# Kernel tuning notes

Measured on AMD Instinct MI355X. Metric: run time of the kernel, lower is better.

Reference implementation:

```python
import jax, jax.numpy as jnp
import numpy as np

B, S, D, H, L, V = 4, 1000, 512, 8, 4, 32000
HD = D // H
FF = 4 * D
EPS = 1e-5


def setup_inputs() -> dict:
    key = jax.random.key(0)
    ks = jax.random.split(key, 24)
    s = 0.02
    inp = {
        'tokens': jax.random.randint(ks[0], (B, S), 0, V, dtype=jnp.int32),
        'emb': jax.random.normal(ks[1], (V, D), jnp.float32) * s,
        'wq': jax.random.normal(ks[2], (L, D, D), jnp.float32) * s,
        'bq': jnp.zeros((L, D), jnp.float32),
        'wk': jax.random.normal(ks[3], (L, D, D), jnp.float32) * s,
        'bk': jnp.zeros((L, D), jnp.float32),
        'wv': jax.random.normal(ks[4], (L, D, D), jnp.float32) * s,
        'bv': jnp.zeros((L, D), jnp.float32),
        'wo': jax.random.normal(ks[5], (L, D, D), jnp.float32) * s,
        'bo': jnp.zeros((L, D), jnp.float32),
        'ln1_g': jnp.ones((L, D), jnp.float32),
        'ln1_b': jnp.zeros((L, D), jnp.float32),
        'w1': jax.random.normal(ks[6], (L, D, FF), jnp.float32) * s,
        'b1': jnp.zeros((L, FF), jnp.float32),
        'w2': jax.random.normal(ks[7], (L, FF, D), jnp.float32) * s,
        'b2': jnp.zeros((L, D), jnp.float32),
        'ln2_g': jnp.ones((L, D), jnp.float32),
        'ln2_b': jnp.zeros((L, D), jnp.float32),
        'fc_w': jax.random.normal(ks[8], (D, V), jnp.float32) * s,
        'fc_b': jnp.zeros((V,), jnp.float32),
    }
    return inp


def _layernorm(x, g, b):
    mu = jnp.mean(x, axis=-1, keepdims=True)
    var = jnp.mean(jnp.square(x - mu), axis=-1, keepdims=True)
    return (x - mu) * jax.lax.rsqrt(var + EPS) * g + b


def _pos_encoding(seq_len, dim):
    pos = jnp.arange(seq_len, dtype=jnp.float32)[:, None]
    div = jnp.exp(jnp.arange(0, dim, 2, dtype=jnp.float32) * (-np.log(10000.0) / dim))
    pe = jnp.zeros((seq_len, dim), jnp.float32)
    pe = pe.at[:, 0::2].set(jnp.sin(pos * div))
    pe = pe.at[:, 1::2].set(jnp.cos(pos * div))
    return pe


def reference(tokens, emb, wq, bq, wk, bk, wv, bv, wo, bo,
              ln1_g, ln1_b, w1, b1, w2, b2, ln2_g, ln2_b, fc_w, fc_b):
    x = emb[tokens]                      # [B,S,D]
    x = x + _pos_encoding(S, D)
    scale = 1.0 / np.sqrt(HD)
    for i in range(L):
        # multi-head attention (unfused, as in source)
        q = (x @ wq[i] + bq[i]).reshape(B, S, H, HD).transpose(0, 2, 1, 3)
        k = (x @ wk[i] + bk[i]).reshape(B, S, H, HD).transpose(0, 2, 1, 3)
        v = (x @ wv[i] + bv[i]).reshape(B, S, H, HD).transpose(0, 2, 1, 3)
        scores = jnp.einsum('bhqd,bhkd->bhqk', q, k) * scale  # [B,H,S,S]
        attn = jax.nn.softmax(scores, axis=-1)
        ctx = jnp.einsum('bhqk,bhkd->bhqd', attn, v)
        ctx = ctx.transpose(0, 2, 1, 3).reshape(B, S, D)
        attended = ctx @ wo[i] + bo[i]
        x = _layernorm(x + attended, ln1_g[i], ln1_b[i])
        # feed-forward
        h = jax.nn.relu(x @ w1[i] + b1[i])
        ff = h @ w2[i] + b2[i]
        x = _layernorm(x + ff, ln2_g[i], ln2_b[i])
    logits = x @ fc_w + fc_b             # [B,S,V]
    return jax.nn.softmax(logits, axis=-1)
```

## Files before the change

kernel.cpp:

```cpp
#include <hip/hip_runtime.h>
#include <math.h>

#define BB 4
#define SS 1000
#define DD 512
#define HH 8
#define HD 64
#define LL 4
#define FFD 2048
#define VV 32000
#define MM (BB*SS)
#define QKV_STR 1536

typedef __attribute__((ext_vector_type(8))) short bf16x8;
typedef __attribute__((ext_vector_type(4))) short bf16x4;
typedef __attribute__((ext_vector_type(4))) float f32x4;

__device__ __forceinline__ unsigned short f2bf(float f)
{
    unsigned int u = __float_as_uint(f);
    u += 0x7FFFu + ((u >> 16) & 1u);
    return (unsigned short)(u >> 16);
}
__device__ __forceinline__ float bf2f(unsigned short h)
{
    return __uint_as_float((unsigned int)h << 16);
}
__device__ __forceinline__ void cvt8(const float* f, unsigned int* hp, unsigned int* lp)
{
#pragma unroll
    for (int j = 0; j < 4; j++) {
        unsigned short h0 = f2bf(f[2 * j]);
        unsigned short h1 = f2bf(f[2 * j + 1]);
        unsigned short l0 = f2bf(f[2 * j] - bf2f(h0));
        unsigned short l1 = f2bf(f[2 * j + 1] - bf2f(h1));
        hp[j] = (unsigned int)h0 | ((unsigned int)h1 << 16);
        lp[j] = (unsigned int)l0 | ((unsigned int)l1 << 16);
    }
}
__device__ __forceinline__ void split8(const float* f, bf16x8& h8, bf16x8& l8)
{
#pragma unroll
    for (int j = 0; j < 8; j++) {
        unsigned short h = f2bf(f[j]);
        unsigned short l = f2bf(f[j] - bf2f(h));
        h8[j] = (short)h;
        l8[j] = (short)l;
    }
}

__global__ __launch_bounds__(256) void embed_pe_kernel(
    const int* __restrict__ tokens, const float* __restrict__ emb,
    float* __restrict__ x)
{
    int idx = blockIdx.x * 256 + threadIdx.x;
    int d  = idx & (DD - 1);
    int bs = idx >> 9;
    int s  = bs % SS;
    int tok = tokens[bs];
    float i2 = (float)(d & ~1);
    float dv = expf(i2 * (-9.210340371976184f / (float)DD));
    float ang = (float)s * dv;
    float pe = (d & 1) ? cosf(ang) : sinf(ang);
    x[idx] = emb[(size_t)tok * DD + d] + pe;
}

#define BKP 40

__device__ __forceinline__ void gemm_core(
    const float* __restrict__ A, const float* __restrict__ W, int ldw, int wcol,
    const float* __restrict__ bias, float* __restrict__ C, int ldc, int ccol,
    int M, int K, int relu, int bm)
{
    __shared__ unsigned short Ah[128][BKP];
    __shared__ unsigned short Al[128][BKP];
    __shared__ unsigned short Bh[128][BKP];
    __shared__ unsigned short Bl[128][BKP];

    const int tid  = threadIdx.x;
    const int lane = tid & 63;
    const int wid  = tid >> 6;
    const int wm   = (wid >> 1) << 6;
    const int wn   = (wid & 1) << 6;
    const int fr   = lane & 15;
    const int ko   = (lane >> 4) << 3;

    const int am  = tid >> 2;
    const int aks = (tid & 3) << 3;
    const int bn  = tid & 63;
    const int bkk = (tid >> 6) << 3;

    f32x4 acc[4][4];
#pragma unroll
    for (int i = 0; i < 4; i++)
#pragma unroll
        for (int j = 0; j < 4; j++)
            acc[i][j] = (f32x4){0.f, 0.f, 0.f, 0.f};

    for (int k0 = 0; k0 < K; k0 += 32) {
#pragma unroll
        for (int u = 0; u < 2; u++) {
            const int m  = am + (u << 6);
            const int gm = bm + m;
            float fv[8];
            if (gm < M) {
                const float* ap = &A[(size_t)gm * K + k0 + aks];
                float4 x0 = *(const float4*)ap;
                float4 x1 = *(const float4*)(ap + 4);
                fv[0] = x0.x; fv[1] = x0.y; fv[2] = x0.z; fv[3] = x0.w;
                fv[4] = x1.x; fv[5] = x1.y; fv[6] = x1.z; fv[7] = x1.w;
            } else {
#pragma unroll
                for (int j = 0; j < 8; j++) fv[j] = 0.f;
            }
            unsigned int hp[4], lp[4];
            cvt8(fv, hp, lp);
            *(uint4*)&Ah[m][aks] = make_uint4(hp[0], hp[1], hp[2], hp[3]);
            *(uint4*)&Al[m][aks] = make_uint4(lp[0], lp[1], lp[2], lp[3]);
        }
#pragma unroll
        for (int u = 0; u < 2; u++) {
            const int n = bn + (u << 6);
            const float* wp = &W[(size_t)(k0 + bkk) * ldw + wcol + n];
            float fv[8];
#pragma unroll
            for (int i = 0; i < 8; i++) fv[i] = wp[(size_t)i * ldw];
            unsigned int hp[4], lp[4];
            cvt8(fv, hp, lp);
            *(uint4*)&Bh[n][bkk] = make_uint4(hp[0], hp[1], hp[2], hp[3]);
            *(uint4*)&Bl[n][bkk] = make_uint4(lp[0], lp[1], lp[2], lp[3]);
        }
        __syncthreads();

        bf16x8 ah[4], al[4], bh[4], bl[4];
#pragma unroll
        for (int i = 0; i < 4; i++) {
            ah[i] = *(const bf16x8*)&Ah[wm + i * 16 + fr][ko];
            al[i] = *(const bf16x8*)&Al[wm + i * 16 + fr][ko];
        }
#pragma unroll
        for (int j = 0; j < 4; j++) {
            bh[j] = *(const bf16x8*)&Bh[wn + j * 16 + fr][ko];
            bl[j] = *(const bf16x8*)&Bl[wn + j * 16 + fr][ko];
        }
#pragma unroll
        for (int i = 0; i < 4; i++)
#pragma unroll
            for (int j = 0; j < 4; j++) {
                acc[i][j] = __builtin_amdgcn_mfma_f32_16x16x32_bf16(ah[i], bh[j], acc[i][j], 0, 0, 0);
                acc[i][j] = __builtin_amdgcn_mfma_f32_16x16x32_bf16(ah[i], bl[j], acc[i][j], 0, 0, 0);
                acc[i][j] = __builtin_amdgcn_mfma_f32_16x16x32_bf16(al[i], bh[j], acc[i][j], 0, 0, 0);
            }
        __syncthreads();
    }

    const int cr = (lane >> 4) << 2;
    const int cc = lane & 15;
#pragma unroll
    for (int j = 0; j < 4; j++) {
        const int lc  = wn + j * 16 + cc;
        const float bv = bias[wcol + lc];
        const int col = ccol + lc;
#pragma unroll
        for (int i = 0; i < 4; i++) {
            f32x4 a = acc[i][j];
#pragma unroll
            for (int r = 0; r < 4; r++) {
                const int row = bm + wm + i * 16 + cr + r;
                if (row < M) {
                    float v = a[r] + bv;
                    if (relu) v = fmaxf(v, 0.f);
                    C[(size_t)row * ldc + col] = v;
                }
            }
        }
    }
}

__global__ __launch_bounds__(256) void gemm_mfma_kernel(
    const float* __restrict__ A, const float* __restrict__ W,
    const float* __restrict__ bias, float* __restrict__ C,
    int M, int N, int K, int relu)
{
    const int bm   = blockIdx.y * 128;
    const int wcol = blockIdx.x * 128;
    gemm_core(A, W, N, wcol, bias, C, N, wcol, M, K, relu, bm);
}

__global__ __launch_bounds__(256) void gemm_qkv_kernel(
    const float* __restrict__ A,
    const float* __restrict__ wq, const float* __restrict__ wk, const float* __restrict__ wv,
    const float* __restrict__ bq, const float* __restrict__ bk, const float* __restrict__ bv,
    float* __restrict__ qkv, int M)
{
    const int bm   = blockIdx.y * 128;
    const int bx   = blockIdx.x;
    const int sel  = bx >> 2;
    const int wcol = (bx & 3) << 7;
    const int ccol = bx << 7;
    const float* W  = (sel == 0) ? wq : (sel == 1) ? wk : wv;
    const float* bi = (sel == 0) ? bq : (sel == 1) ? bk : bv;
    gemm_core(A, W, DD, wcol, bi, qkv, QKV_STR, ccol, M, DD, 0, bm);
}

#define QT 128
#define KVT 64
#define KP 72
#define VP 72

__device__ __forceinline__ bf16x8 ld_pair(const unsigned short* p0,
                                          const unsigned short* p1)
{
    union { bf16x8 v; bf16x4 q[2]; } u;
    u.q[0] = *(const bf16x4*)p0;
    u.q[1] = *(const bf16x4*)p1;
    return u.v;
}

__global__ __launch_bounds__(512) void attention_kernel(
    const float* __restrict__ qkv, float* __restrict__ ctx)
{
    __shared__ __align__(16) unsigned short Kh[KVT][KP];
    __shared__ __align__(16) unsigned short Kl[KVT][KP];
    __shared__ __align__(16) unsigned short Vth[HD][VP];
    __shared__ __align__(16) unsigned short Vtl[HD][VP];

    const int tid  = threadIdx.x;
    const int lane = tid & 63;
    const int w    = tid >> 6;
    const int r16  = lane & 15;
    const int g    = lane >> 4;

    const int nqt = (SS + QT - 1) / QT;
    const int qt  = blockIdx.x % nqt;
    const int bh  = blockIdx.x / nqt;
    const int h   = bh % HH;
    const int b   = bh / HH;
    const int q0  = qt * QT;

    const size_t base = (size_t)b * SS * QKV_STR + (size_t)h * HD;

    const int qrow = q0 + w * 16 + r16;
    const int qr   = qrow < SS ? qrow : SS - 1;
    const float* qp = qkv + base + (size_t)qr * QKV_STR;
    bf16x8 qh[2], ql[2];
#pragma unroll
    for (int c = 0; c < 2; c++) {
        float4 qa = *(const float4*)&qp[c * 32 + g * 4];
        float4 qb = *(const float4*)&qp[c * 32 + 16 + g * 4];
        float fv[8] = {qa.x * 0.125f, qa.y * 0.125f, qa.z * 0.125f, qa.w * 0.125f,
                       qb.x * 0.125f, qb.y * 0.125f, qb.z * 0.125f, qb.w * 0.125f};
        split8(fv, qh[c], ql[c]);
    }

    f32x4 oacc[4];
#pragma unroll
    for (int f = 0; f < 4; f++) oacc[f] = (f32x4){0.f, 0.f, 0.f, 0.f};
    float mrow = -1e30f, lrow = 0.f;

    const int ntiles = (SS + KVT - 1) / KVT;
    for (int t = 0; t < ntiles; t++) {
        const int kv0 = t * KVT;
        __syncthreads();
        {
            const int kj   = tid >> 3;
            const int dblk = (tid & 7) * 8;
            float fv[8];
            const int krow = kv0 + kj;
            if (krow < SS) {
                const float* kp = qkv + base + (size_t)krow * QKV_STR + DD;
                float4 a0 = *(const float4*)&kp[dblk];
                float4 a1 = *(const float4*)&kp[dblk + 4];
                fv[0] = a0.x; fv[1] = a0.y; fv[2] = a0.z; fv[3] = a0.w;
                fv[4] = a1.x; fv[5] = a1.y; fv[6] = a1.z; fv[7] = a1.w;
            } else {
#pragma unroll
                for (int j = 0; j < 8; j++) fv[j] = 0.f;
            }
            bf16x8 h8, l8;
            split8(fv, h8, l8);
            *(bf16x8*)&Kh[kj][dblk] = h8;
            *(bf16x8*)&Kl[kj][dblk] = l8;
        }
        {
            const int kj = tid & 63;
            const int d0 = (tid >> 6) * 8;
            float fv[8];
            const int vrow = kv0 + kj;
            if (vrow < SS) {
                const float* vp = qkv + base + (size_t)vrow * QKV_STR + 2 * DD;
                float4 a0 = *(const float4*)&vp[d0];
                float4 a1 = *(const float4*)&vp[d0 + 4];
                fv[0] = a0.x; fv[1] = a0.y; fv[2] = a0.z; fv[3] = a0.w;
                fv[4] = a1.x; fv[5] = a1.y; fv[6] = a1.z; fv[7] = a1.w;
            } else {
#pragma unroll
                for (int j = 0; j < 8; j++) fv[j] = 0.f;
            }
#pragma unroll
            for (int i = 0; i < 8; i++) {
                unsigned short hh = f2bf(fv[i]);
                unsigned short ll = f2bf(fv[i] - bf2f(hh));
                Vth[d0 + i][kj] = hh;
                Vtl[d0 + i][kj] = ll;
            }
        }
        __syncthreads();

        f32x4 sac[4];
#pragma unroll
        for (int f = 0; f < 4; f++) sac[f] = (f32x4){0.f, 0.f, 0.f, 0.f};
#pragma unroll
        for (int f = 0; f < 4; f++) {
            const int ar = f * 16 + r16;
#pragma unroll
            for (int c = 0; c < 2; c++) {
                bf16x8 ah = ld_pair(&Kh[ar][c * 32 + g * 4], &Kh[ar][c * 32 + 16 + g * 4]);
                bf16x8 al = ld_pair(&Kl[ar][c * 32 + g * 4], &Kl[ar][c * 32 + 16 + g * 4]);
                sac[f] = __builtin_amdgcn_mfma_f32_16x16x32_bf16(ah, qh[c], sac[f], 0, 0, 0);
                sac[f] = __builtin_amdgcn_mfma_f32_16x16x32_bf16(ah, ql[c], sac[f], 0, 0, 0);
                sac[f] = __builtin_amdgcn_mfma_f32_16x16x32_bf16(al, qh[c], sac[f], 0, 0, 0);
            }
        }
        if (kv0 + KVT > SS) {
#pragma unroll
            for (int f = 0; f < 4; f++)
#pragma unroll
                for (int rr = 0; rr < 4; rr++)
                    if (kv0 + f * 16 + g * 4 + rr >= SS) sac[f][rr] = -1e30f;
        }

        float tmax = -1e30f;
#pragma unroll
        for (int f = 0; f < 4; f++)
#pragma unroll
            for (int rr = 0; rr < 4; rr++) tmax = fmaxf(tmax, sac[f][rr]);
        tmax = fmaxf(tmax, __shfl_xor(tmax, 16));
        tmax = fmaxf(tmax, __shfl_xor(tmax, 32));
        const float mnew = fmaxf(mrow, tmax);
        const float scal = __expf(mrow - mnew);
        mrow = mnew;
        float tsum = 0.f;
#pragma unroll
        for (int f = 0; f < 4; f++)
#pragma unroll
            for (int rr = 0; rr < 4; rr++) {
                float e = __expf(sac[f][rr] - mnew);
                sac[f][rr] = e;
                tsum += e;
            }
        tsum += __shfl_xor(tsum, 16);
        tsum += __shfl_xor(tsum, 32);
        lrow = lrow * scal + tsum;
#pragma unroll
        for (int f = 0; f < 4; f++) {
            oacc[f][0] *= scal; oacc[f][1] *= scal;
            oacc[f][2] *= scal; oacc[f][3] *= scal;
        }

        bf16x8 ph[2], pl[2];
#pragma unroll
        for (int c = 0; c < 2; c++) {
            float pv[8] = {sac[2 * c][0], sac[2 * c][1], sac[2 * c][2], sac[2 * c][3],
                           sac[2 * c + 1][0], sac[2 * c + 1][1], sac[2 * c + 1][2], sac[2 * c + 1][3]};
            split8(pv, ph[c], pl[c]);
        }

#pragma unroll
        for (int f = 0; f < 4; f++) {
            const int ar = f * 16 + r16;
#pragma unroll
            for (int c = 0; c < 2; c++) {
                bf16x8 vh = ld_pair(&Vth[ar][c * 32 + g * 4], &Vth[ar][c * 32 + 16 + g * 4]);
                bf16x8 vl = ld_pair(&Vtl[ar][c * 32 + g * 4], &Vtl[ar][c * 32 + 16 + g * 4]);
                oacc[f] = __builtin_amdgcn_mfma_f32_16x16x32_bf16(vh, ph[c], oacc[f], 0, 0, 0);
                oacc[f] = __builtin_amdgcn_mfma_f32_16x16x32_bf16(vh, pl[c], oacc[f], 0, 0, 0);
                oacc[f] = __builtin_amdgcn_mfma_f32_16x16x32_bf16(vl, ph[c], oacc[f], 0, 0, 0);
            }
        }
    }

    if (qrow < SS) {
        const float inv = 1.f / lrow;
        float* cp = ctx + ((size_t)b * SS + qrow) * DD + (size_t)h * HD;
#pragma unroll
        for (int f = 0; f < 4; f++) {
            float4 o;
            o.x = oacc[f][0] * inv;
            o.y = oacc[f][1] * inv;
            o.z = oacc[f][2] * inv;
            o.w = oacc[f][3] * inv;
            *(float4*)&cp[f * 16 + g * 4] = o;
        }
    }
}

__global__ __launch_bounds__(128) void add_ln_kernel(
    float* __restrict__ x, const float* __restrict__ res,
    const float* __restrict__ g, const float* __restrict__ bta)
{
    const int row = blockIdx.x;
    const int tid = threadIdx.x;
    float* xr = x + (size_t)row * DD;
    const float* rr = res + (size_t)row * DD;

    float4 xv = ((const float4*)xr)[tid];
    float4 rv = ((const float4*)rr)[tid];
    xv.x += rv.x; xv.y += rv.y; xv.z += rv.z; xv.w += rv.w;

    __shared__ float red1[2];
    __shared__ float red2[2];
    const int lane = tid & 63;
    const int w = tid >> 6;

    float s = xv.x + xv.y + xv.z + xv.w;
#pragma unroll
    for (int off = 32; off > 0; off >>= 1) s += __shfl_xor(s, off);
    if (lane == 0) red1[w] = s;
    __syncthreads();
    const float mean = (red1[0] + red1[1]) * (1.f / (float)DD);

    float d0 = xv.x - mean, d1 = xv.y - mean, d2 = xv.z - mean, d3 = xv.w - mean;
    float sq = d0 * d0 + d1 * d1 + d2 * d2 + d3 * d3;
#pragma unroll
    for (int off = 32; off > 0; off >>= 1) sq += __shfl_xor(sq, off);
    if (lane == 0) red2[w] = sq;
    __syncthreads();
    const float inv = 1.f / sqrtf((red2[0] + red2[1]) * (1.f / (float)DD) + 1e-5f);

    float4 gv = ((const float4*)g)[tid];
    float4 bv = ((const float4*)bta)[tid];
    float4 o;
    o.x = d0 * inv * gv.x + bv.x;
    o.y = d1 * inv * gv.y + bv.y;
    o.z = d2 * inv * gv.z + bv.z;
    o.w = d3 * inv * gv.w + bv.w;
    ((float4*)xr)[tid] = o;
}

__global__ __launch_bounds__(256) void softmax_kernel(float* __restrict__ out)
{
    const int row = blockIdx.x;
    float* p = out + (size_t)row * VV;
    const int tid = threadIdx.x;

    float m = -1e30f, s = 0.f;
    for (int j = tid * 4; j < VV; j += 1024) {
        float4 c = *(const float4*)&p[j];
        float lm = fmaxf(fmaxf(c.x, c.y), fmaxf(c.z, c.w));
        if (lm > m) { s *= expf(m - lm); m = lm; }
        s += expf(c.x - m) + expf(c.y - m) + expf(c.z - m) + expf(c.w - m);
    }
#pragma unroll
    for (int off = 32; off > 0; off >>= 1) {
        float mo = __shfl_xor(m, off);
        float so = __shfl_xor(s, off);
        float nm = fmaxf(m, mo);
        s = s * expf(m - nm) + so * expf(mo - nm);
        m = nm;
    }
    __shared__ float ms[4], ss2[4];
    const int lane = tid & 63;
    const int w = tid >> 6;
    if (lane == 0) { ms[w] = m; ss2[w] = s; }
    __syncthreads();
    float fm = fmaxf(fmaxf(ms[0], ms[1]), fmaxf(ms[2], ms[3]));
    float fs = ss2[0] * expf(ms[0] - fm) + ss2[1] * expf(ms[1] - fm) +
               ss2[2] * expf(ms[2] - fm) + ss2[3] * expf(ms[3] - fm);
    const float inv = 1.f / fs;
    for (int j = tid * 4; j < VV; j += 1024) {
        float4 c = *(const float4*)&p[j];
        c.x = expf(c.x - fm) * inv;
        c.y = expf(c.y - fm) * inv;
        c.z = expf(c.z - fm) * inv;
        c.w = expf(c.w - fm) * inv;
        *(float4*)&p[j] = c;
    }
}

static inline void launch_gemm(const float* A, const float* W, const float* bias,
                               float* C, int M, int N, int K, int relu,
                               hipStream_t st)
{
    dim3 grid(N / 128, (M + 127) / 128);
    gemm_mfma_kernel<<<grid, 256, 0, st>>>(A, W, bias, C, M, N, K, relu);
}

extern "C" void kernel_launch(void* const* d_in, const int* in_sizes, int n_in,
                              void* d_out, int out_size, void* d_ws, size_t ws_size,
                              hipStream_t stream)
{
    const int*   tokens = (const int*)  d_in[0];
    const float* emb    = (const float*)d_in[1];
    const float* wq     = (const float*)d_in[2];
    const float* bq     = (const float*)d_in[3];
    const float* wk     = (const float*)d_in[4];
    const float* bk     = (const float*)d_in[5];
    const float* wv     = (const float*)d_in[6];
    const float* bv     = (const float*)d_in[7];
    const float* wo     = (const float*)d_in[8];
    const float* bo     = (const float*)d_in[9];
    const float* ln1g   = (const float*)d_in[10];
    const float* ln1b   = (const float*)d_in[11];
    const float* w1     = (const float*)d_in[12];
    const float* b1     = (const float*)d_in[13];
    const float* w2     = (const float*)d_in[14];
    const float* b2     = (const float*)d_in[15];
    const float* ln2g   = (const float*)d_in[16];
    const float* ln2b   = (const float*)d_in[17];
    const float* fcw    = (const float*)d_in[18];
    const float* fcb    = (const float*)d_in[19];
    float* out = (float*)d_out;

    const size_t XN = (size_t)MM * DD;
    float* x    = (float*)d_ws;
    float* qkv  = x   + XN;
    float* ctx  = qkv + 3 * XN;
    float* attn = ctx + XN;
    float* hbuf = out + ((size_t)MM * VV - (size_t)MM * FFD);

    embed_pe_kernel<<<(MM * DD) / 256, 256, 0, stream>>>(tokens, emb, x);

    for (int l = 0; l < LL; l++) {
        const size_t wo2 = (size_t)l * DD * DD;
        gemm_qkv_kernel<<<dim3(12, (MM + 127) / 128), 256, 0, stream>>>(
            x, wq + wo2, wk + wo2, wv + wo2,
            bq + l * DD, bk + l * DD, bv + l * DD, qkv, MM);
        attention_kernel<<<BB * HH * ((SS + QT - 1) / QT), 512, 0, stream>>>(qkv, ctx);
        launch_gemm(ctx, wo + wo2, bo + l * DD, attn, MM, DD, DD, 0, stream);
        add_ln_kernel<<<MM, 128, 0, stream>>>(x, attn, ln1g + l * DD, ln1b + l * DD);
        launch_gemm(x, w1 + (size_t)l * DD * FFD, b1 + l * FFD, hbuf, MM, FFD, DD, 1, stream);
        launch_gemm(hbuf, w2 + (size_t)l * FFD * DD, b2 + l * DD, attn, MM, DD, FFD, 0, stream);
        add_ln_kernel<<<MM, 128, 0, stream>>>(x, attn, ln2g + l * DD, ln2b + l * DD);
    }

    launch_gemm(x, fcw, fcb, out, MM, VV, DD, 0, stream);
    softmax_kernel<<<MM, 256, 0, stream>>>(out);
}
```

Measured before the change: 2.942 ms.

## Pre-split activations and weights to bf16 hi/lo, drop split for final projection

Producers (embedding, layernorm, GEMM epilogues, attention) now write bf16 hi/lo pairs directly, and weights are pre-transposed and split by a separate conversion kernel. GEMMs and attention load bf16 tiles straight into shared memory instead of converting fp32 on every tile load. The large vocabulary projection now uses a single bf16 MFMA pass with bf16-only activations instead of the 3-term split. This removes repeated conversion work and the strided weight reads, but the output GEMM loses the lo correction terms, which lowers logits precision.

```diff
diff --git a/kernel.cpp b/kernel.cpp
--- a/kernel.cpp
+++ b/kernel.cpp
@@ -26,18 +26,6 @@
 {
     return __uint_as_float((unsigned int)h << 16);
 }
-__device__ __forceinline__ void cvt8(const float* f, unsigned int* hp, unsigned int* lp)
-{
-#pragma unroll
-    for (int j = 0; j < 4; j++) {
-        unsigned short h0 = f2bf(f[2 * j]);
-        unsigned short h1 = f2bf(f[2 * j + 1]);
-        unsigned short l0 = f2bf(f[2 * j] - bf2f(h0));
-        unsigned short l1 = f2bf(f[2 * j + 1] - bf2f(h1));
-        hp[j] = (unsigned int)h0 | ((unsigned int)h1 << 16);
-        lp[j] = (unsigned int)l0 | ((unsigned int)l1 << 16);
-    }
-}
 __device__ __forceinline__ void split8(const float* f, bf16x8& h8, bf16x8& l8)
 {
 #pragma unroll
@@ -51,7 +39,8 @@
 
 __global__ __launch_bounds__(256) void embed_pe_kernel(
     const int* __restrict__ tokens, const float* __restrict__ emb,
-    float* __restrict__ x)
+    float* __restrict__ x, unsigned short* __restrict__ xhi,
+    unsigned short* __restrict__ xlo)
 {
     int idx = blockIdx.x * 256 + threadIdx.x;
     int d  = idx & (DD - 1);
@@ -62,20 +51,76 @@
     float dv = expf(i2 * (-9.210340371976184f / (float)DD));
     float ang = (float)s * dv;
     float pe = (d & 1) ? cosf(ang) : sinf(ang);
-    x[idx] = emb[(size_t)tok * DD + d] + pe;
+    float v = emb[(size_t)tok * DD + d] + pe;
+    x[idx] = v;
+    unsigned short h = f2bf(v);
+    xhi[idx] = h;
+    xlo[idx] = f2bf(v - bf2f(h));
+}
+
+__global__ __launch_bounds__(256) void wtconv_kernel(
+    const float* __restrict__ W, int ldn,
+    unsigned short* __restrict__ thi, unsigned short* __restrict__ tlo,
+    int ldk, int n0)
+{
+    __shared__ unsigned short lh[32][33];
+    __shared__ unsigned short ll[32][33];
+    const int tid = threadIdx.x;
+    const int nn0 = blockIdx.x * 32;
+    const int k0  = blockIdx.y * 32;
+
+    {
+        const int k = tid >> 3;
+        const int n = (tid & 7) * 4;
+        float4 v = *(const float4*)&W[(size_t)(k0 + k) * ldn + nn0 + n];
+        float fv[4] = {v.x, v.y, v.z, v.w};
+#pragma unroll
+        for (int i = 0; i < 4; i++) {
+            unsigned short h = f2bf(fv[i]);
+            lh[k][n + i] = h;
+            ll[k][n + i] = f2bf(fv[i] - bf2f(h));
+        }
+    }
+    __syncthreads();
+    {
+        const int nw = tid >> 3;
+        const int kw = (tid & 7) * 4;
+        unsigned int h0 = (unsigned int)lh[kw][nw]     | ((unsigned int)lh[kw + 1][nw] << 16);
+        unsigned int h1 = (unsigned int)lh[kw + 2][nw] | ((unsigned int)lh[kw + 3][nw] << 16);
+        unsigned int l0 = (unsigned int)ll[kw][nw]     | ((unsigned int)ll[kw + 1][nw] << 16);
+        unsigned int l1 = (unsigned int)ll[kw + 2][nw] | ((unsigned int)ll[kw + 3][nw] << 16);
+        const size_t o = (size_t)(n0 + nn0 + nw) * ldk + k0 + kw;
+        *(uint2*)&thi[o] = make_uint2(h0, h1);
+        *(uint2*)&tlo[o] = make_uint2(l0, l1);
+    }
+}
+
+__global__ __launch_bounds__(256) void concat_bias_kernel(
+    const float* __restrict__ a, const float* __restrict__ b,
+    const float* __restrict__ c, float* __restrict__ o)
+{
+    int t = blockIdx.x * 256 + threadIdx.x;
+    if (t < 512) o[t] = a[t];
+    else if (t < 1024) o[t] = b[t - 512];
+    else if (t < 1536) o[t] = c[t - 1024];
 }
 
 #define BKP 40
 
-__device__ __forceinline__ void gemm_core(
-    const float* __restrict__ A, const float* __restrict__ W, int ldw, int wcol,
-    const float* __restrict__ bias, float* __restrict__ C, int ldc, int ccol,
-    int M, int K, int relu, int bm)
+template<int SPLIT, bool BF32, bool OSPLIT>
+__global__ __launch_bounds__(256) void gemm_t(
+    const unsigned short* __restrict__ Ahi, const unsigned short* __restrict__ Alo,
+    const unsigned short* __restrict__ Bth, const unsigned short* __restrict__ Btl,
+    const float* __restrict__ Bf, int ldbf,
+    const float* __restrict__ bias,
+    float* __restrict__ Cf, unsigned short* __restrict__ Chi,
+    unsigned short* __restrict__ Clo,
+    int M, int K, int ldc, int relu)
 {
     __shared__ unsigned short Ah[128][BKP];
-    __shared__ unsigned short Al[128][BKP];
+    __shared__ unsigned short Al[SPLIT == 3 ? 128 : 1][SPLIT == 3 ? BKP : 1];
     __shared__ unsigned short Bh[128][BKP];
-    __shared__ unsigned short Bl[128][BKP];
+    __shared__ unsigned short Bl[SPLIT == 3 ? 128 : 1][SPLIT == 3 ? BKP : 1];
 
     const int tid  = threadIdx.x;
     const int lane = tid & 63;
@@ -84,11 +129,8 @@
     const int wn   = (wid & 1) << 6;
     const int fr   = lane & 15;
     const int ko   = (lane >> 4) << 3;
-
-    const int am  = tid >> 2;
-    const int aks = (tid & 3) << 3;
-    const int bn  = tid & 63;
-    const int bkk = (tid >> 6) << 3;
+    const int bm   = blockIdx.y * 128;
+    const int bn0  = blockIdx.x * 128;
 
     f32x4 acc[4][4];
 #pragma unroll
@@ -97,59 +139,63 @@
         for (int j = 0; j < 4; j++)
             acc[i][j] = (f32x4){0.f, 0.f, 0.f, 0.f};
 
+    const uint4 zz = {0u, 0u, 0u, 0u};
     for (int k0 = 0; k0 < K; k0 += 32) {
 #pragma unroll
-        for (int u = 0; u < 2; u++) {
-            const int m  = am + (u << 6);
-            const int gm = bm + m;
-            float fv[8];
-            if (gm < M) {
-                const float* ap = &A[(size_t)gm * K + k0 + aks];
-                float4 x0 = *(const float4*)ap;
-                float4 x1 = *(const float4*)(ap + 4);
-                fv[0] = x0.x; fv[1] = x0.y; fv[2] = x0.z; fv[3] = x0.w;
-                fv[4] = x1.x; fv[5] = x1.y; fv[6] = x1.z; fv[7] = x1.w;
-            } else {
-#pragma unroll
-                for (int j = 0; j < 8; j++) fv[j] = 0.f;
-            }
-            unsigned int hp[4], lp[4];
-            cvt8(fv, hp, lp);
-            *(uint4*)&Ah[m][aks] = make_uint4(hp[0], hp[1], hp[2], hp[3]);
-            *(uint4*)&Al[m][aks] = make_uint4(lp[0], lp[1], lp[2], lp[3]);
-        }
-#pragma unroll
-        for (int u = 0; u < 2; u++) {
-            const int n = bn + (u << 6);
-            const float* wp = &W[(size_t)(k0 + bkk) * ldw + wcol + n];
-            float fv[8];
-#pragma unroll
-            for (int i = 0; i < 8; i++) fv[i] = wp[(size_t)i * ldw];
-            unsigned int hp[4], lp[4];
-            cvt8(fv, hp, lp);
-            *(uint4*)&Bh[n][bkk] = make_uint4(hp[0], hp[1], hp[2], hp[3]);
-            *(uint4*)&Bl[n][bkk] = make_uint4(lp[0], lp[1], lp[2], lp[3]);
+        for (int p = 0; p < 2; p++) {
+            const int c   = tid + (p << 8);
+            const int row = c >> 2;
+            const int ks  = (c & 3) << 3;
+            const int gm  = bm + row;
+            *(uint4*)&Ah[row][ks] =
+                (gm < M) ? *(const uint4*)&Ahi[(size_t)gm * K + k0 + ks] : zz;
+            if (SPLIT == 3)
+                *(uint4*)&Al[row][ks] =
+                    (gm < M) ? *(const uint4*)&Alo[(size_t)gm * K + k0 + ks] : zz;
+            if (!BF32) {
+                *(uint4*)&Bh[row][ks] = *(const uint4*)&Bth[(size_t)(bn0 + row) * K + k0 + ks];
+                if (SPLIT == 3)
+                    *(uint4*)&Bl[row][ks] = *(const uint4*)&Btl[(size_t)(bn0 + row) * K + k0 + ks];
+            }
+        }
+        if (BF32) {
+#pragma unroll
+            for (int u = 0; u < 2; u++) {
+                const int n   = (tid & 63) + (u << 6);
+                const int bkk = (tid >> 6) << 3;
+                const float* wp = &Bf[(size_t)(k0 + bkk) * ldbf + bn0 + n];
+                unsigned int hp[4];
+#pragma unroll
+                for (int i = 0; i < 4; i++) {
+                    unsigned short h0 = f2bf(wp[(size_t)(2 * i) * ldbf]);
+                    unsigned short h1 = f2bf(wp[(size_t)(2 * i + 1) * ldbf]);
+                    hp[i] = (unsigned int)h0 | ((unsigned int)h1 << 16);
+                }
+                *(uint4*)&Bh[n][bkk] = make_uint4(hp[0], hp[1], hp[2], hp[3]);
+            }
         }
         __syncthreads();
 
-        bf16x8 ah[4], al[4], bh[4], bl[4];
+        bf16x8 ah[4], bh[4], al[4], bl[4];
 #pragma unroll
         for (int i = 0; i < 4; i++) {
             ah[i] = *(const bf16x8*)&Ah[wm + i * 16 + fr][ko];
-            al[i] = *(const bf16x8*)&Al[wm + i * 16 + fr][ko];
+            if (SPLIT == 3) al[i] = *(const bf16x8*)&Al[wm + i * 16 + fr][ko];
         }
 #pragma unroll
         for (int j = 0; j < 4; j++) {
             bh[j] = *(const bf16x8*)&Bh[wn + j * 16 + fr][ko];
-            bl[j] = *(const bf16x8*)&Bl[wn + j * 16 + fr][ko];
+            if (SPLIT == 3) bl[j] = *(const bf16x8*)&Bl[wn + j * 16 + fr][ko];
         }
 #pragma unroll
         for (int i = 0; i < 4; i++)
 #pragma unroll
             for (int j = 0; j < 4; j++) {
                 acc[i][j] = __builtin_amdgcn_mfma_f32_16x16x32_bf16(ah[i], bh[j], acc[i][j], 0, 0, 0);
-                acc[i][j] = __builtin_amdgcn_mfma_f32_16x16x32_bf16(ah[i], bl[j], acc[i][j], 0, 0, 0);
-                acc[i][j] = __builtin_amdgcn_mfma_f32_16x16x32_bf16(al[i], bh[j], acc[i][j], 0, 0, 0);
+                if (SPLIT == 3) {
+                    acc[i][j] = __builtin_amdgcn_mfma_f32_16x16x32_bf16(ah[i], bl[j], acc[i][j], 0, 0, 0);
+                    acc[i][j] = __builtin_amdgcn_mfma_f32_16x16x32_bf16(al[i], bh[j], acc[i][j], 0, 0, 0);
+                }
             }
         __syncthreads();
     }
@@ -159,8 +205,8 @@
 #pragma unroll
     for (int j = 0; j < 4; j++) {
         const int lc  = wn + j * 16 + cc;
-        const float bv = bias[wcol + lc];
-        const int col = ccol + lc;
+        const float bv = bias[bn0 + lc];
+        const int col = bn0 + lc;
 #pragma unroll
         for (int i = 0; i < 4; i++) {
             f32x4 a = acc[i][j];
@@ -170,37 +216,17 @@
                 if (row < M) {
                     float v = a[r] + bv;
                     if (relu) v = fmaxf(v, 0.f);
-                    C[(size_t)row * ldc + col] = v;
+                    if (OSPLIT) {
+                        unsigned short h = f2bf(v);
+                        Chi[(size_t)row * ldc + col] = h;
+                        Clo[(size_t)row * ldc + col] = f2bf(v - bf2f(h));
+                    } else {
+                        Cf[(size_t)row * ldc + col] = v;
+                    }
                 }
             }
         }
     }
-}
-
-__global__ __launch_bounds__(256) void gemm_mfma_kernel(
-    const float* __restrict__ A, const float* __restrict__ W,
-    const float* __restrict__ bias, float* __restrict__ C,
-    int M, int N, int K, int relu)
-{
-    const int bm   = blockIdx.y * 128;
-    const int wcol = blockIdx.x * 128;
-    gemm_core(A, W, N, wcol, bias, C, N, wcol, M, K, relu, bm);
-}
-
-__global__ __launch_bounds__(256) void gemm_qkv_kernel(
-    const float* __restrict__ A,
-    const float* __restrict__ wq, const float* __restrict__ wk, const float* __restrict__ wv,
-    const float* __restrict__ bq, const float* __restrict__ bk, const float* __restrict__ bv,
-    float* __restrict__ qkv, int M)
-{
-    const int bm   = blockIdx.y * 128;
-    const int bx   = blockIdx.x;
-    const int sel  = bx >> 2;
-    const int wcol = (bx & 3) << 7;
-    const int ccol = bx << 7;
-    const float* W  = (sel == 0) ? wq : (sel == 1) ? wk : wv;
-    const float* bi = (sel == 0) ? bq : (sel == 1) ? bk : bv;
-    gemm_core(A, W, DD, wcol, bi, qkv, QKV_STR, ccol, M, DD, 0, bm);
 }
 
 #define QT 128
@@ -218,7 +244,8 @@
 }
 
 __global__ __launch_bounds__(512) void attention_kernel(
-    const float* __restrict__ qkv, float* __restrict__ ctx)
+    const unsigned short* __restrict__ qvh, const unsigned short* __restrict__ qvl,
+    unsigned short* __restrict__ chi, unsigned short* __restrict__ clo)
 {
     __shared__ __align__(16) unsigned short Kh[KVT][KP];
     __shared__ __align__(16) unsigned short Kl[KVT][KP];
@@ -242,15 +269,13 @@
 
     const int qrow = q0 + w * 16 + r16;
     const int qr   = qrow < SS ? qrow : SS - 1;
-    const float* qp = qkv + base + (size_t)qr * QKV_STR;
+    const unsigned short* qph = qvh + base + (size_t)qr * QKV_STR;
+    const unsigned short* qpl = qvl + base + (size_t)qr * QKV_STR;
     bf16x8 qh[2], ql[2];
 #pragma unroll
     for (int c = 0; c < 2; c++) {
-        float4 qa = *(const float4*)&qp[c * 32 + g * 4];
-        float4 qb = *(const float4*)&qp[c * 32 + 16 + g * 4];
-        float fv[8] = {qa.x * 0.125f, qa.y * 0.125f, qa.z * 0.125f, qa.w * 0.125f,
-                       qb.x * 0.125f, qb.y * 0.125f, qb.z * 0.125f, qb.w * 0.125f};
-        split8(fv, qh[c], ql[c]);
+        qh[c] = ld_pair(&qph[c * 32 + g * 4], &qph[c * 32 + 16 + g * 4]);
+        ql[c] = ld_pair(&qpl[c * 32 + g * 4], &qpl[c * 32 + 16 + g * 4]);
     }
 
     f32x4 oacc[4];
@@ -258,6 +283,7 @@
     for (int f = 0; f < 4; f++) oacc[f] = (f32x4){0.f, 0.f, 0.f, 0.f};
     float mrow = -1e30f, lrow = 0.f;
 
+    const uint4 zz = {0u, 0u, 0u, 0u};
     const int ntiles = (SS + KVT - 1) / KVT;
     for (int t = 0; t < ntiles; t++) {
         const int kv0 = t * KVT;
@@ -265,44 +291,32 @@
         {
             const int kj   = tid >> 3;
             const int dblk = (tid & 7) * 8;
-            float fv[8];
             const int krow = kv0 + kj;
             if (krow < SS) {
-                const float* kp = qkv + base + (size_t)krow * QKV_STR + DD;
-                float4 a0 = *(const float4*)&kp[dblk];
-                float4 a1 = *(const float4*)&kp[dblk + 4];
-                fv[0] = a0.x; fv[1] = a0.y; fv[2] = a0.z; fv[3] = a0.w;
-                fv[4] = a1.x; fv[5] = a1.y; fv[6] = a1.z; fv[7] = a1.w;
+                const size_t o = base + (size_t)krow * QKV_STR + DD + dblk;
+                *(uint4*)&Kh[kj][dblk] = *(const uint4*)&qvh[o];
+                *(uint4*)&Kl[kj][dblk] = *(const uint4*)&qvl[o];
             } else {
-#pragma unroll
-                for (int j = 0; j < 8; j++) fv[j] = 0.f;
-            }
-            bf16x8 h8, l8;
-            split8(fv, h8, l8);
-            *(bf16x8*)&Kh[kj][dblk] = h8;
-            *(bf16x8*)&Kl[kj][dblk] = l8;
+                *(uint4*)&Kh[kj][dblk] = zz;
+                *(uint4*)&Kl[kj][dblk] = zz;
+            }
         }
         {
             const int kj = tid & 63;
             const int d0 = (tid >> 6) * 8;
-            float fv[8];
             const int vrow = kv0 + kj;
+            union { uint4 u; unsigned short s[8]; } vh4, vl4;
             if (vrow < SS) {
-                const float* vp = qkv + base + (size_t)vrow * QKV_STR + 2 * DD;
-                float4 a0 = *(const float4*)&vp[d0];
-                float4 a1 = *(const float4*)&vp[d0 + 4];
-                fv[0] = a0.x; fv[1] = a0.y; fv[2] = a0.z; fv[3] = a0.w;
-                fv[4] = a1.x; fv[5] = a1.y; fv[6] = a1.z; fv[7] = a1.w;
+                const size_t o = base + (size_t)vrow * QKV_STR + 2 * DD + d0;
+                vh4.u = *(const uint4*)&qvh[o];
+                vl4.u = *(const uint4*)&qvl[o];
             } else {
-#pragma unroll
-                for (int j = 0; j < 8; j++) fv[j] = 0.f;
+                vh4.u = zz; vl4.u = zz;
             }
 #pragma unroll
             for (int i = 0; i < 8; i++) {
-                unsigned short hh = f2bf(fv[i]);
-                unsigned short ll = f2bf(fv[i] - bf2f(hh));
-                Vth[d0 + i][kj] = hh;
-                Vtl[d0 + i][kj] = ll;
+                Vth[d0 + i][kj] = vh4.s[i];
+                Vtl[d0 + i][kj] = vl4.s[i];
             }
         }
         __syncthreads();
@@ -322,6 +336,10 @@
                 sac[f] = __builtin_amdgcn_mfma_f32_16x16x32_bf16(al, qh[c], sac[f], 0, 0, 0);
             }
         }
+#pragma unroll
+        for (int f = 0; f < 4; f++)
+#pragma unroll
+            for (int rr = 0; rr < 4; rr++) sac[f][rr] *= 0.125f;
         if (kv0 + KVT > SS) {
 #pragma unroll
             for (int f = 0; f < 4; f++)
@@ -382,22 +400,30 @@
 
     if (qrow < SS) {
         const float inv = 1.f / lrow;
-        float* cp = ctx + ((size_t)b * SS + qrow) * DD + (size_t)h * HD;
+        const size_t ci = ((size_t)b * SS + qrow) * DD + (size_t)h * HD;
 #pragma unroll
         for (int f = 0; f < 4; f++) {
-            float4 o;
-            o.x = oacc[f][0] * inv;
-            o.y = oacc[f][1] * inv;
-            o.z = oacc[f][2] * inv;
-            o.w = oacc[f][3] * inv;
-            *(float4*)&cp[f * 16 + g * 4] = o;
+            unsigned short hs[4], ls[4];
+#pragma unroll
+            for (int r = 0; r < 4; r++) {
+                float v = oacc[f][r] * inv;
+                hs[r] = f2bf(v);
+                ls[r] = f2bf(v - bf2f(hs[r]));
+            }
+            unsigned int h0 = (unsigned int)hs[0] | ((unsigned int)hs[1] << 16);
+            unsigned int h1 = (unsigned int)hs[2] | ((unsigned int)hs[3] << 16);
+            unsigned int l0 = (unsigned int)ls[0] | ((unsigned int)ls[1] << 16);
+            unsigned int l1 = (unsigned int)ls[2] | ((unsigned int)ls[3] << 16);
+            *(uint2*)&chi[ci + f * 16 + g * 4] = make_uint2(h0, h1);
+            *(uint2*)&clo[ci + f * 16 + g * 4] = make_uint2(l0, l1);
         }
     }
 }
 
 __global__ __launch_bounds__(128) void add_ln_kernel(
     float* __restrict__ x, const float* __restrict__ res,
-    const float* __restrict__ g, const float* __restrict__ bta)
+    const float* __restrict__ g, const float* __restrict__ bta,
+    unsigned short* __restrict__ xhi, unsigned short* __restrict__ xlo)
 {
     const int row = blockIdx.x;
     const int tid = threadIdx.x;
@@ -436,6 +462,15 @@
     o.z = d2 * inv * gv.z + bv.z;
     o.w = d3 * inv * gv.w + bv.w;
     ((float4*)xr)[tid] = o;
+
+    unsigned short h0 = f2bf(o.x), h1 = f2bf(o.y), h2 = f2bf(o.z), h3 = f2bf(o.w);
+    unsigned short l0 = f2bf(o.x - bf2f(h0)), l1 = f2bf(o.y - bf2f(h1));
+    unsigned short l2 = f2bf(o.z - bf2f(h2)), l3 = f2bf(o.w - bf2f(h3));
+    const size_t oidx = (size_t)row * DD + tid * 4;
+    *(uint2*)&xhi[oidx] = make_uint2((unsigned int)h0 | ((unsigned int)h1 << 16),
+                                     (unsigned int)h2 | ((unsigned int)h3 << 16));
+    *(uint2*)&xlo[oidx] = make_uint2((unsigned int)l0 | ((unsigned int)l1 << 16),
+                                     (unsigned int)l2 | ((unsigned int)l3 << 16));
 }
 
 __global__ __launch_bounds__(256) void softmax_kernel(float* __restrict__ out)
@@ -476,14 +511,6 @@
         c.w = expf(c.w - fm) * inv;
         *(float4*)&p[j] = c;
     }
-}
-
-static inline void launch_gemm(const float* A, const float* W, const float* bias,
-                               float* C, int M, int N, int K, int relu,
-                               hipStream_t st)
-{
-    dim3 grid(N / 128, (M + 127) / 128);
-    gemm_mfma_kernel<<<grid, 256, 0, st>>>(A, W, bias, C, M, N, K, relu);
 }
 
 extern "C" void kernel_launch(void* const* d_in, const int* in_sizes, int n_in,
@@ -513,27 +540,57 @@
     float* out = (float*)d_out;
 
     const size_t XN = (size_t)MM * DD;
-    float* x    = (float*)d_ws;
-    float* qkv  = x   + XN;
-    float* ctx  = qkv + 3 * XN;
-    float* attn = ctx + XN;
-    float* hbuf = out + ((size_t)MM * VV - (size_t)MM * FFD);
-
-    embed_pe_kernel<<<(MM * DD) / 256, 256, 0, stream>>>(tokens, emb, x);
+    float* ws = (float*)d_ws;
+    float* x = ws;
+    unsigned short* xhi = (unsigned short*)(ws + XN);
+    unsigned short* xlo = xhi + XN;
+    unsigned short* qkvhi = (unsigned short*)(ws + 2 * XN);
+    unsigned short* qkvlo = qkvhi + 3 * XN;
+    float* attn = ws + 5 * XN;
+
+    unsigned short* tailu = (unsigned short*)(out + ((size_t)MM * VV - (size_t)MM * FFD));
+    unsigned short* ctxhi = tailu;
+    unsigned short* ctxlo = tailu + XN;
+    unsigned short* Hhi   = tailu;
+    unsigned short* Hlo   = tailu + (size_t)MM * FFD;
+
+    unsigned short* wth = qkvhi;
+    unsigned short* wtl = qkvhi + 1048576;
+    unsigned short* qwth = (unsigned short*)attn;
+    unsigned short* qwtl = qwth + 786432;
+    float* biasc = (float*)(qwtl + 786432);
+
+    embed_pe_kernel<<<(MM * DD) / 256, 256, 0, stream>>>(tokens, emb, x, xhi, xlo);
 
     for (int l = 0; l < LL; l++) {
         const size_t wo2 = (size_t)l * DD * DD;
-        gemm_qkv_kernel<<<dim3(12, (MM + 127) / 128), 256, 0, stream>>>(
-            x, wq + wo2, wk + wo2, wv + wo2,
-            bq + l * DD, bk + l * DD, bv + l * DD, qkv, MM);
-        attention_kernel<<<BB * HH * ((SS + QT - 1) / QT), 512, 0, stream>>>(qkv, ctx);
-        launch_gemm(ctx, wo + wo2, bo + l * DD, attn, MM, DD, DD, 0, stream);
-        add_ln_kernel<<<MM, 128, 0, stream>>>(x, attn, ln1g + l * DD, ln1b + l * DD);
-        launch_gemm(x, w1 + (size_t)l * DD * FFD, b1 + l * FFD, hbuf, MM, FFD, DD, 1, stream);
-        launch_gemm(hbuf, w2 + (size_t)l * FFD * DD, b2 + l * DD, attn, MM, DD, FFD, 0, stream);
-        add_ln_kernel<<<MM, 128, 0, stream>>>(x, attn, ln2g + l * DD, ln2b + l * DD);
-    }
-
-    launch_gemm(x, fcw, fcb, out, MM, VV, DD, 0, stream);
+        concat_bias_kernel<<<6, 256, 0, stream>>>(bq + l * DD, bk + l * DD, bv + l * DD, biasc);
+        wtconv_kernel<<<dim3(16, 16), 256, 0, stream>>>(wq + wo2, DD, qwth, qwtl, DD, 0);
+        wtconv_kernel<<<dim3(16, 16), 256, 0, stream>>>(wk + wo2, DD, qwth, qwtl, DD, 512);
+        wtconv_kernel<<<dim3(16, 16), 256, 0, stream>>>(wv + wo2, DD, qwth, qwtl, DD, 1024);
+        gemm_t<3, false, true><<<dim3(12, 32), 256, 0, stream>>>(
+            xhi, xlo, qwth, qwtl, nullptr, 0, biasc,
+            nullptr, qkvhi, qkvlo, MM, DD, QKV_STR, 0);
+        attention_kernel<<<BB * HH * ((SS + QT - 1) / QT), 512, 0, stream>>>(
+            qkvhi, qkvlo, ctxhi, ctxlo);
+        wtconv_kernel<<<dim3(16, 16), 256, 0, stream>>>(wo + wo2, DD, wth, wtl, DD, 0);
+        gemm_t<3, false, false><<<dim3(4, 32), 256, 0, stream>>>(
+            ctxhi, ctxlo, wth, wtl, nullptr, 0, bo + l * DD,
+            attn, nullptr, nullptr, MM, DD, DD, 0);
+        add_ln_kernel<<<MM, 128, 0, stream>>>(x, attn, ln1g + l * DD, ln1b + l * DD, xhi, xlo);
+        wtconv_kernel<<<dim3(64, 16), 256, 0, stream>>>(w1 + (size_t)l * DD * FFD, FFD, wth, wtl, DD, 0);
+        gemm_t<3, false, true><<<dim3(16, 32), 256, 0, stream>>>(
+            xhi, xlo, wth, wtl, nullptr, 0, b1 + l * FFD,
+            nullptr, Hhi, Hlo, MM, DD, FFD, 1);
+        wtconv_kernel<<<dim3(16, 64), 256, 0, stream>>>(w2 + (size_t)l * FFD * DD, DD, wth, wtl, FFD, 0);
+        gemm_t<3, false, false><<<dim3(4, 32), 256, 0, stream>>>(
+            Hhi, Hlo, wth, wtl, nullptr, 0, b2 + l * DD,
+            attn, nullptr, nullptr, MM, FFD, DD, 0);
+        add_ln_kernel<<<MM, 128, 0, stream>>>(x, attn, ln2g + l * DD, ln2b + l * DD, xhi, xlo);
+    }
+
+    gemm_t<1, true, false><<<dim3(VV / 128, 32), 256, 0, stream>>>(
+        xhi, nullptr, nullptr, nullptr, fcw, VV, fcb,
+        out, nullptr, nullptr, MM, DD, VV, 0);
     softmax_kernel<<<MM, 256, 0, stream>>>(out);
 }
```

After: 2.770 ms. 5.8% less time.
